# Kernel optimization log

Measured on AMD Instinct MI355X. Metric: run time of the kernel, lower is better.

The kernel has to match this reference:

```python
import jax, jax.numpy as jnp
import numpy as np

VOCAB = 50000
D_EMB = 300
N_BINS = 11
B, LQ, LD = 64, 32, 1024
MU = np.array([1.0, 0.9, 0.7, 0.5, 0.3, 0.1, -0.1, -0.3, -0.5, -0.7, -0.9], dtype=np.float32)
SIGMA = np.array([1e-3] + [0.1] * 10, dtype=np.float32)


def setup_inputs() -> dict:
    key = jax.random.key(0)
    ks = jax.random.split(key, 8)
    inputs_q = jax.random.randint(ks[0], (B, LQ), 0, VOCAB, dtype=jnp.int64 if jax.config.jax_enable_x64 else jnp.int32)
    inputs_d = jax.random.randint(ks[1], (B, LD), 0, VOCAB, dtype=jnp.int64 if jax.config.jax_enable_x64 else jnp.int32)
    mask_q = jnp.ones((B, LQ), dtype=jnp.float32)
    mask_d = jnp.ones((B, LD), dtype=jnp.float32)
    word_emb = jax.random.normal(ks[2], (VOCAB, D_EMB), dtype=jnp.float32) * 0.1
    attn_table = jax.random.uniform(ks[3], (VOCAB, 1), dtype=jnp.float32)  # frozen IDF embedding
    idf_w = jax.random.normal(ks[4], (1, 1), dtype=jnp.float32)
    idf_b = jnp.zeros((1,), dtype=jnp.float32)
    dense_w = jax.random.normal(ks[5], (1, N_BINS), dtype=jnp.float32) * 0.1
    dense_b = jnp.zeros((1,), dtype=jnp.float32)
    return {
        'inputs_q': inputs_q, 'inputs_d': inputs_d,
        'mask_q': mask_q, 'mask_d': mask_d,
        'word_emb': word_emb, 'attn_table': attn_table,
        'idf_w': idf_w, 'idf_b': idf_b,
        'dense_w': dense_w, 'dense_b': dense_b,
    }


def _l2_normalize(x, eps=1e-12):
    # matches F.normalize(x, 2, dim=-1): x / max(||x||, eps)
    n = jnp.sqrt(jnp.sum(x * x, axis=-1, keepdims=True))
    return x / jnp.maximum(n, eps)


def reference(inputs_q, inputs_d, mask_q, mask_d, word_emb, attn_table,
              idf_w, idf_b, dense_w, dense_b):
    mu = jnp.asarray(MU)        # [K]
    sigma = jnp.asarray(SIGMA)  # [K]
    # idf attention on query tokens: Linear(1,1) on frozen embedding lookup
    attn_q = attn_table[inputs_q] * idf_w[0, 0] + idf_b[0]          # [B,Lq,1]
    q_embed = _l2_normalize(word_emb[inputs_q])                      # [B,Lq,E]
    d_embed = _l2_normalize(word_emb[inputs_d])                      # [B,Ld,E]
    sim = jnp.einsum('bqe,bde->bqd', q_embed, d_embed)               # [B,Lq,Ld]
    # RBF soft-histogram over n_bins kernels, doc tokens masked
    rbf = jnp.exp(-((sim[..., None] - mu) ** 2) / (sigma ** 2) / 2)  # [B,Lq,Ld,K]
    pooling_sum = jnp.einsum('bqdk,bd->bqk', rbf, mask_d)            # [B,Lq,K]
    wq = mask_q[..., None] * attn_q                                   # [B,Lq,1]
    log_pool = jnp.log(jnp.clip(pooling_sum, 1e-10)) * wq * 0.01     # [B,Lq,K]
    log_pooling_sum = jnp.sum(log_pool, axis=1)                      # [B,K]
    out = jnp.tanh(log_pooling_sum @ dense_w.T + dense_b)            # [B,1]
    return out[:, 0]                                                 # [B]
```

## Files before the change

### kernel.cpp

```cpp
#include <hip/hip_runtime.h>
#include <math.h>

#define VOCAB  50000
#define D_EMB  300
#define NBINS  11
#define BATCH  64
#define LQ     32
#define LD     1024
#define NSTEP  10
#define DT2    32
#define NDT2   (LD / DT2)

#define PARTIAL2_BYTES ((size_t)NDT2 * BATCH * LQ * NBINS * 4)

typedef __attribute__((ext_vector_type(8))) short short8;
typedef __attribute__((ext_vector_type(4))) float floatx4;

__constant__ float c_mu[NBINS]  = {1.0f, 0.9f, 0.7f, 0.5f, 0.3f, 0.1f,
                                   -0.1f, -0.3f, -0.5f, -0.7f, -0.9f};
__constant__ float c_is2[NBINS] = {500000.0f, 50.f, 50.f, 50.f, 50.f, 50.f,
                                   50.f, 50.f, 50.f, 50.f, 50.f};

static __device__ __forceinline__ unsigned short f32_bf16(float f) {
  unsigned u = __float_as_uint(f);
  u += 0x7FFFu + ((u >> 16) & 1u);
  return (unsigned short)(u >> 16);
}
static __device__ __forceinline__ float bf16_f32(unsigned short h) {
  return __uint_as_float(((unsigned)h) << 16);
}

static __device__ __forceinline__ short8 cvt8(float4 fa, float4 fb, float& p) {
  unsigned short h[8];
  h[0] = f32_bf16(fa.x); h[1] = f32_bf16(fa.y);
  h[2] = f32_bf16(fa.z); h[3] = f32_bf16(fa.w);
  h[4] = f32_bf16(fb.x); h[5] = f32_bf16(fb.y);
  h[6] = f32_bf16(fb.z); h[7] = f32_bf16(fb.w);
  short8 v;
#pragma unroll
  for (int j = 0; j < 8; ++j) {
    const float x = bf16_f32(h[j]);
    p += x * x;
    v[j] = (short)h[j];
  }
  return v;
}

__global__ __launch_bounds__(256) void knrm_main3(
    const int* __restrict__ inputs_q, const int* __restrict__ inputs_d,
    const float* __restrict__ mask_d, const float* __restrict__ word_emb,
    float* __restrict__ partial)
{
  const int b    = blockIdx.y;
  const int dt   = blockIdx.x;
  const int tid  = threadIdx.x;
  const int wid  = tid >> 6;
  const int lane = tid & 63;
  const int khi  = lane >> 4;
  const int rl   = lane & 15;
  const int qt   = wid >> 1, dp = wid & 1;

  __shared__ float red[4][16][NBINS];

  const int dbase = b * LD + dt * DT2;
  const int qtok  = inputs_q[b * LQ + qt * 16 + rl];
  const int dtok  = inputs_d[dbase + dp * 16 + rl];
  const float* qrow = word_emb + (size_t)qtok * D_EMB;
  const float* drow = word_emb + (size_t)dtok * D_EMB;

  short8 afr[NSTEP], bfr[NSTEP];
  float pq = 0.f, pd = 0.f;
#pragma unroll
  for (int s = 0; s < NSTEP; ++s) {
    const int k0 = 32 * s + 8 * khi;
    float4 fa = make_float4(0.f, 0.f, 0.f, 0.f);
    float4 fb = make_float4(0.f, 0.f, 0.f, 0.f);
    if (k0 < D_EMB)     fa = *(const float4*)(qrow + k0);
    if (k0 + 4 < D_EMB) fb = *(const float4*)(qrow + k0 + 4);
    afr[s] = cvt8(fa, fb, pq);
  }
#pragma unroll
  for (int s = 0; s < NSTEP; ++s) {
    const int k0 = 32 * s + 8 * khi;
    float4 fa = make_float4(0.f, 0.f, 0.f, 0.f);
    float4 fb = make_float4(0.f, 0.f, 0.f, 0.f);
    if (k0 < D_EMB)     fa = *(const float4*)(drow + k0);
    if (k0 + 4 < D_EMB) fb = *(const float4*)(drow + k0 + 4);
    bfr[s] = cvt8(fa, fb, pd);
  }
  pq += __shfl_xor(pq, 16); pq += __shfl_xor(pq, 32);
  pd += __shfl_xor(pd, 16); pd += __shfl_xor(pd, 32);
  const float invq_own = 1.f / fmaxf(sqrtf(pq), 1e-12f);
  const float invd     = 1.f / fmaxf(sqrtf(pd), 1e-12f);

  floatx4 acc = {0.f, 0.f, 0.f, 0.f};
#pragma unroll
  for (int s = 0; s < NSTEP; ++s)
    acc = __builtin_amdgcn_mfma_f32_16x16x32_bf16(afr[s], bfr[s], acc, 0, 0, 0);

  float iq[4];
#pragma unroll
  for (int r = 0; r < 4; ++r) iq[r] = __shfl(invq_own, 4 * khi + r);

  const float md = mask_d[dbase + dp * 16 + rl];
  float ps[4][NBINS];
#pragma unroll
  for (int r = 0; r < 4; ++r) {
    const float sv = acc[r] * iq[r] * invd;
#pragma unroll
    for (int k = 0; k < NBINS; ++k) {
      const float d = sv - c_mu[k];
      ps[r][k] = md * __expf(-d * d * c_is2[k]);
    }
  }

#pragma unroll
  for (int off = 1; off < 16; off <<= 1)
#pragma unroll
    for (int r = 0; r < 4; ++r)
#pragma unroll
      for (int k = 0; k < NBINS; ++k)
        ps[r][k] += __shfl_xor(ps[r][k], off);

  if (rl == 0)
#pragma unroll
    for (int r = 0; r < 4; ++r)
#pragma unroll
      for (int k = 0; k < NBINS; ++k)
        red[wid][4 * khi + r][k] = ps[r][k];
  __syncthreads();

  float* pout = partial + ((size_t)dt * BATCH + b) * (LQ * NBINS);
  for (int v = tid; v < LQ * NBINS; v += 256) {
    const int q = v / NBINS, k = v % NBINS;
    pout[v] = (q < 16) ? (red[0][q][k] + red[1][q][k])
                       : (red[2][q - 16][k] + red[3][q - 16][k]);
  }
}

__global__ __launch_bounds__(128) void knrm_finalize(
    const float* __restrict__ partial, const int* __restrict__ inputs_q,
    const float* __restrict__ mask_q, const float* __restrict__ attn_table,
    const float* __restrict__ idf_w, const float* __restrict__ idf_b,
    const float* __restrict__ dense_w, const float* __restrict__ dense_b,
    float* __restrict__ out)
{
  const int b   = blockIdx.x;
  const int tid = threadIdx.x;
  __shared__ float pool[LQ][NBINS];
  __shared__ float wq_s[LQ];
  __shared__ float lps[NBINS];

  for (int v = tid; v < LQ * NBINS; v += 128) {
    float s = 0.f;
#pragma unroll
    for (int t = 0; t < NDT2; ++t)
      s += partial[((size_t)t * BATCH + b) * (LQ * NBINS) + v];
    pool[v / NBINS][v % NBINS] = logf(fmaxf(s, 1e-10f));
  }
  if (tid < LQ) {
    const int tok = inputs_q[b * LQ + tid];
    wq_s[tid] = mask_q[b * LQ + tid] * (attn_table[tok] * idf_w[0] + idf_b[0]);
  }
  __syncthreads();
  if (tid < NBINS) {
    float s = 0.f;
    for (int q = 0; q < LQ; ++q) s += pool[q][tid] * wq_s[q];
    lps[tid] = 0.01f * s;
  }
  __syncthreads();
  if (tid == 0) {
    float z = dense_b[0];
    for (int k = 0; k < NBINS; ++k) z += lps[k] * dense_w[k];
    out[b] = tanhf(z);
  }
}

extern "C" void kernel_launch(void* const* d_in, const int* in_sizes, int n_in,
                              void* d_out, int out_size, void* d_ws, size_t ws_size,
                              hipStream_t stream) {
  const int*   inputs_q  = (const int*)d_in[0];
  const int*   inputs_d  = (const int*)d_in[1];
  const float* mask_q    = (const float*)d_in[2];
  const float* mask_d    = (const float*)d_in[3];
  const float* word_emb  = (const float*)d_in[4];
  const float* attn_tab  = (const float*)d_in[5];
  const float* idf_w     = (const float*)d_in[6];
  const float* idf_b     = (const float*)d_in[7];
  const float* dense_w   = (const float*)d_in[8];
  const float* dense_b   = (const float*)d_in[9];
  float* out     = (float*)d_out;
  float* partial = (float*)d_ws;

  dim3 grid(NDT2, BATCH);
  knrm_main3<<<grid, 256, 0, stream>>>(inputs_q, inputs_d, mask_d, word_emb, partial);
  knrm_finalize<<<BATCH, 128, 0, stream>>>(partial, inputs_q, mask_q, attn_tab,
                                           idf_w, idf_b, dense_w, dense_b, out);
}
```

Measured before the change: 144.4 us.

## Pre-convert embedding table to padded bf16 and load fragments via global_load_lds

```diff
diff --git a/kernel.cpp b/kernel.cpp
--- a/kernel.cpp
+++ b/kernel.cpp
@@ -8,13 +8,20 @@
 #define LQ     32
 #define LD     1024
 #define NSTEP  10
+#define KPAD   320
 #define DT2    32
 #define NDT2   (LD / DT2)
 
-#define PARTIAL2_BYTES ((size_t)NDT2 * BATCH * LQ * NBINS * 4)
+#define PARTIAL_BYTES ((size_t)NDT2 * BATCH * LQ * NBINS * 4)
+#define TB_OFF        ((size_t)3 * 1024 * 1024)
+#define TB_BYTES      ((size_t)VOCAB * KPAD * 2)
+#define INV_OFF       (TB_OFF + TB_BYTES)
+#define WS_NEED       (INV_OFF + (size_t)VOCAB * 4)
 
 typedef __attribute__((ext_vector_type(8))) short short8;
 typedef __attribute__((ext_vector_type(4))) float floatx4;
+typedef __attribute__((ext_vector_type(4))) unsigned short us4;
+typedef unsigned int u32;
 
 __constant__ float c_mu[NBINS]  = {1.0f, 0.9f, 0.7f, 0.5f, 0.3f, 0.1f,
                                    -0.1f, -0.3f, -0.5f, -0.7f, -0.9f};
@@ -28,6 +35,130 @@
 }
 static __device__ __forceinline__ float bf16_f32(unsigned short h) {
   return __uint_as_float(((unsigned)h) << 16);
+}
+
+static __device__ __forceinline__ void gload_lds16(const void* g, void* l) {
+  __builtin_amdgcn_global_load_lds(
+      (__attribute__((address_space(1))) u32*)g,
+      (__attribute__((address_space(3))) u32*)l, 16, 0, 0);
+}
+
+__global__ __launch_bounds__(256) void knrm_prep(
+    const float* __restrict__ word_emb,
+    unsigned short* __restrict__ tb, float* __restrict__ invn)
+{
+  const int wid  = threadIdx.x >> 6;
+  const int lane = threadIdx.x & 63;
+  const int row  = blockIdx.x * 4 + wid;
+  if (row >= VOCAB) return;
+  const float4* src = (const float4*)(word_emb + (size_t)row * D_EMB);
+  const float4 a = src[lane];
+  float4 c = make_float4(0.f, 0.f, 0.f, 0.f);
+  if (lane < 11) c = src[64 + lane];
+  us4 ha, hc;
+  ha.x = f32_bf16(a.x); ha.y = f32_bf16(a.y);
+  ha.z = f32_bf16(a.z); ha.w = f32_bf16(a.w);
+  hc.x = f32_bf16(c.x); hc.y = f32_bf16(c.y);
+  hc.z = f32_bf16(c.z); hc.w = f32_bf16(c.w);
+  float p = 0.f;
+  { float x;
+    x = bf16_f32(ha.x); p += x * x;  x = bf16_f32(ha.y); p += x * x;
+    x = bf16_f32(ha.z); p += x * x;  x = bf16_f32(ha.w); p += x * x;
+    x = bf16_f32(hc.x); p += x * x;  x = bf16_f32(hc.y); p += x * x;
+    x = bf16_f32(hc.z); p += x * x;  x = bf16_f32(hc.w); p += x * x; }
+#pragma unroll
+  for (int off = 1; off < 64; off <<= 1) p += __shfl_xor(p, off);
+  unsigned short* orow = tb + (size_t)row * KPAD;
+  *(us4*)(orow + 4 * lane) = ha;
+  if (lane < 16) *(us4*)(orow + 256 + 4 * lane) = hc;
+  if (lane == 0) invn[row] = 1.f / fmaxf(sqrtf(p), 1e-12f);
+}
+
+__global__ __launch_bounds__(256) void knrm_main5(
+    const int* __restrict__ inputs_q, const int* __restrict__ inputs_d,
+    const float* __restrict__ mask_d, const unsigned short* __restrict__ tb,
+    const float* __restrict__ invn, float* __restrict__ partial)
+{
+  const int b    = blockIdx.y;
+  const int dt   = blockIdx.x;
+  const int tid  = threadIdx.x;
+  const int wid  = tid >> 6;
+  const int lane = tid & 63;
+  const int khi  = lane >> 4;
+  const int rl   = lane & 15;
+
+  __shared__ __align__(16) short Afrag[2 * NSTEP * 512];
+  __shared__ __align__(16) short Bfrag[2 * NSTEP * 512];
+  __shared__ float red[4][16][NBINS];
+
+  const int dbase = b * LD + dt * DT2;
+
+  {
+    int tok;
+    char* dst;
+    if (wid < 2) { tok = inputs_q[b * LQ + wid * 16 + rl];
+                   dst = (char*)(Afrag + wid * (NSTEP * 512)); }
+    else         { tok = inputs_d[dbase + (wid - 2) * 16 + rl];
+                   dst = (char*)(Bfrag + (wid - 2) * (NSTEP * 512)); }
+    const char* src = (const char*)tb + (size_t)tok * (KPAD * 2) + khi * 16;
+#pragma unroll
+    for (int s = 0; s < NSTEP; ++s)
+      gload_lds16(src + 64 * s, dst + s * 1024);
+  }
+
+  const int qt = wid >> 1, dp = wid & 1;
+  const float invq_own = invn[inputs_q[b * LQ + qt * 16 + rl]];
+  const float invd     = invn[inputs_d[dbase + dp * 16 + rl]];
+  const float md       = mask_d[dbase + dp * 16 + rl];
+  __syncthreads();
+
+  const short* Ab = Afrag + qt * (NSTEP * 512);
+  const short* Bb = Bfrag + dp * (NSTEP * 512);
+  floatx4 acc = {0.f, 0.f, 0.f, 0.f};
+#pragma unroll
+  for (int s = 0; s < NSTEP; ++s) {
+    const short8 a  = *(const short8*)(Ab + s * 512 + lane * 8);
+    const short8 bf = *(const short8*)(Bb + s * 512 + lane * 8);
+    acc = __builtin_amdgcn_mfma_f32_16x16x32_bf16(a, bf, acc, 0, 0, 0);
+  }
+
+  float iq[4];
+#pragma unroll
+  for (int r = 0; r < 4; ++r) iq[r] = __shfl(invq_own, 4 * khi + r);
+
+  float ps[4][NBINS];
+#pragma unroll
+  for (int r = 0; r < 4; ++r) {
+    const float sv = acc[r] * iq[r] * invd;
+#pragma unroll
+    for (int k = 0; k < NBINS; ++k) {
+      const float d = sv - c_mu[k];
+      ps[r][k] = md * __expf(-d * d * c_is2[k]);
+    }
+  }
+
+#pragma unroll
+  for (int off = 1; off < 16; off <<= 1)
+#pragma unroll
+    for (int r = 0; r < 4; ++r)
+#pragma unroll
+      for (int k = 0; k < NBINS; ++k)
+        ps[r][k] += __shfl_xor(ps[r][k], off);
+
+  if (rl == 0)
+#pragma unroll
+    for (int r = 0; r < 4; ++r)
+#pragma unroll
+      for (int k = 0; k < NBINS; ++k)
+        red[wid][4 * khi + r][k] = ps[r][k];
+  __syncthreads();
+
+  float* pout = partial + ((size_t)dt * BATCH + b) * (LQ * NBINS);
+  for (int v = tid; v < LQ * NBINS; v += 256) {
+    const int q = v / NBINS, k = v % NBINS;
+    pout[v] = (q < 16) ? (red[0][q][k] + red[1][q][k])
+                       : (red[2][q - 16][k] + red[3][q - 16][k]);
+  }
 }
 
 static __device__ __forceinline__ short8 cvt8(float4 fa, float4 fb, float& p) {
@@ -193,7 +324,14 @@
   float* partial = (float*)d_ws;
 
   dim3 grid(NDT2, BATCH);
-  knrm_main3<<<grid, 256, 0, stream>>>(inputs_q, inputs_d, mask_d, word_emb, partial);
+  if (ws_size >= WS_NEED) {
+    unsigned short* tb = (unsigned short*)((char*)d_ws + TB_OFF);
+    float* invn        = (float*)((char*)d_ws + INV_OFF);
+    knrm_prep<<<VOCAB / 4, 256, 0, stream>>>(word_emb, tb, invn);
+    knrm_main5<<<grid, 256, 0, stream>>>(inputs_q, inputs_d, mask_d, tb, invn, partial);
+  } else {
+    knrm_main3<<<grid, 256, 0, stream>>>(inputs_q, inputs_d, mask_d, word_emb, partial);
+  }
   knrm_finalize<<<BATCH, 128, 0, stream>>>(partial, inputs_q, mask_q, attn_tab,
                                            idf_w, idf_b, dense_w, dense_b, out);
 }
```

Result: no change. 142.0 us (-1.7%).
